# Kernel optimization log

Hardware: AMD Instinct MI355X
Metric: run time of the kernel (lower is better)

## Reference

```python
import jax, jax.numpy as jnp
import numpy as np

B, T, V, E, H, HD, L, K = 64, 512, 50000, 512, 512, 256, 2, 16
START, STOP, PAD = 13, 14, 15
NEG = -10000.0


def setup_inputs() -> dict:
    key = jax.random.key(0)
    ks = jax.random.split(key, 12)
    x = jax.random.randint(ks[0], (B, T), 0, V, dtype=jnp.int32)
    emb_table = jax.random.normal(ks[1], (V, E), jnp.float32) * 0.1
    w_ih = jax.random.normal(ks[2], (L, 2, 4 * HD, E), jnp.float32) * 0.05
    w_hh = jax.random.normal(ks[3], (L, 2, 4 * HD, HD), jnp.float32) * 0.05
    b_ih = jax.random.normal(ks[4], (L, 2, 4 * HD), jnp.float32) * 0.05
    b_hh = jax.random.normal(ks[5], (L, 2, 4 * HD), jnp.float32) * 0.05
    h0 = jax.random.normal(ks[6], (2 * L, B, HD), jnp.float32)
    c0 = jax.random.normal(ks[7], (2 * L, B, HD), jnp.float32)
    w_out = jax.random.normal(ks[8], (K, H), jnp.float32) * 0.05
    b_out = jax.random.normal(ks[9], (K,), jnp.float32) * 0.05
    t = jax.random.normal(ks[10], (K, K), jnp.float32)
    # replicate the in-place edits (order matters: pad overrides stop/start crossings)
    t = t.at[START, :].set(NEG)
    t = t.at[:, STOP].set(NEG)
    t = t.at[PAD, :].set(0.0)
    t = t.at[:, PAD].set(0.0)
    return {"x": x, "seq_len": T, "emb_table": emb_table, "w_ih": w_ih,
            "w_hh": w_hh, "b_ih": b_ih, "b_hh": b_hh, "h0": h0, "c0": c0,
            "w_out": w_out, "b_out": b_out, "transition": t}


def _lstm_dir(xs, h0, c0, Wih, Whh, b):
    # xs: [B, T, in]; single-direction LSTM, torch gate order (i, f, g, o)
    def step(carry, x_t):
        h, c = carry
        gates = x_t @ Wih.T + h @ Whh.T + b  # [B, 4*HD]
        i, f, g, o = jnp.split(gates, 4, axis=-1)
        c = jax.nn.sigmoid(f) * c + jax.nn.sigmoid(i) * jnp.tanh(g)
        h = jax.nn.sigmoid(o) * jnp.tanh(c)
        return (h, c), h
    _, hs = jax.lax.scan(step, (h0, c0), jnp.swapaxes(xs, 0, 1))  # [T, B, HD]
    return jnp.swapaxes(hs, 0, 1)


def _log_exp_sum(vec):
    # faithful to the original: per-row max over last dim, but sum of exp over ALL elements
    m = jnp.max(vec, axis=-1)
    return m + jnp.log(jnp.sum(jnp.exp(vec - m[..., None])))


def reference(x, seq_len, emb_table, w_ih, w_hh, b_ih, b_hh, h0, c0, w_out, b_out, transition):
    out = emb_table[x]  # [B, T, E]
    for l in range(L):
        fwd = _lstm_dir(out, h0[2 * l], c0[2 * l], w_ih[l, 0], w_hh[l, 0], b_ih[l, 0] + b_hh[l, 0])
        bwd = _lstm_dir(out[:, ::-1], h0[2 * l + 1], c0[2 * l + 1], w_ih[l, 1], w_hh[l, 1], b_ih[l, 1] + b_hh[l, 1])[:, ::-1]
        out = jnp.concatenate([fwd, bwd], axis=-1)  # [B, T, H]
    tag_scores = out @ w_out.T + b_out  # [B, T, K]

    # CRF forward algorithm (vectorized form of the nested time/tag loops)
    alpha0 = jnp.full((B, K), NEG, dtype=tag_scores.dtype).at[:, START].set(0.0)

    def crf_step(alpha, feat_t):  # feat_t: [B, K]
        vec = alpha[:, None, :] + feat_t[:, :, None] + transition[None, :, :]  # [B, Knext, Kprev]
        m = jnp.max(vec, axis=-1)  # [B, Knext]
        # original log_exp_sum sums exp over the whole [B, Kprev] slice per next_tag
        s = jnp.sum(jnp.exp(vec - m[..., None]), axis=(0, 2))  # [Knext]
        return m + jnp.log(s)[None, :], None

    alpha, _ = jax.lax.scan(crf_step, alpha0, jnp.swapaxes(tag_scores, 0, 1))
    terminal = alpha + transition[STOP][None, :]
    forward_score = _log_exp_sum(terminal)  # [B]
    return tag_scores, forward_score
```

## Files before the change

kernel.cpp:

```cpp
#include <hip/hip_runtime.h>

#define B_ 64
#define T_ 512
#define E_ 512
#define HD_ 256
#define H_ 512
#define K_ 16
#define NEG_ (-10000.0f)
#define START_ 13
#define STOP_ 14

typedef unsigned int u32;
using half8  = __attribute__((ext_vector_type(8))) _Float16;
using f32x4  = __attribute__((ext_vector_type(4))) float;
using half2v = __attribute__((ext_vector_type(2))) _Float16;

__device__ __forceinline__ int dot4i8(u32 a, u32 b, int c) {
#if __has_builtin(__builtin_amdgcn_sdot4)
    return __builtin_amdgcn_sdot4((int)a, (int)b, c, false);
#else
    int r = c;
#pragma unroll
    for (int i = 0; i < 4; ++i) {
        int xa = ((int)a << (24 - 8 * i)) >> 24;
        int xb = ((int)b << (24 - 8 * i)) >> 24;
        r += xa * xb;
    }
    return r;
#endif
}
__device__ __forceinline__ int dotq(uint4 w, uint4 h, int a) {
    a = dot4i8(w.x, h.x, a); a = dot4i8(w.y, h.y, a);
    a = dot4i8(w.z, h.z, a); a = dot4i8(w.w, h.w, a);
    return a;
}
__device__ __forceinline__ float sigm(float x) { return 1.f / (1.f + __expf(-x)); }
__device__ __forceinline__ float tanh_f(float x) {
    float a = fabsf(x);
    float e = __expf(-2.f * a);
    float t = (1.f - e) / (1.f + e);
    return x < 0.f ? -t : t;
}

__global__ void cvt_f16_k(const float* __restrict__ src, _Float16* __restrict__ dst, int n4) {
    int i = blockIdx.x * blockDim.x + threadIdx.x;
    if (i < n4) {
        float4 v = ((const float4*)src)[i];
        half2v a; a.x = (_Float16)v.x; a.y = (_Float16)v.y;
        half2v b; b.x = (_Float16)v.z; b.y = (_Float16)v.w;
        ((u32*)dst)[2 * i]     = __builtin_bit_cast(u32, a);
        ((u32*)dst)[2 * i + 1] = __builtin_bit_cast(u32, b);
    }
}
__global__ void bias_sum_k(const float* __restrict__ bih, const float* __restrict__ bhh,
                           float* __restrict__ bs) {
    int i = blockIdx.x * blockDim.x + threadIdx.x;
    if (i < 4096) bs[i] = bih[i] + bhh[i];
}

__global__ void quant_whh_k(const float* __restrict__ whh,
                            u32* __restrict__ wq,
                            float* __restrict__ dqw) {
    const int row = blockIdx.x, lane = threadIdx.x;
    const float4 v = ((const float4*)(whh + (size_t)row * 256))[lane];
    float m = fmaxf(fmaxf(fabsf(v.x), fabsf(v.y)), fmaxf(fabsf(v.z), fabsf(v.w)));
#pragma unroll
    for (int off = 32; off >= 1; off >>= 1) m = fmaxf(m, __shfl_xor(m, off, 64));
    m = fmaxf(m, 1e-8f);
    const float s = 127.f / m;
    int b0 = ((int)rintf(v.x * s)) & 255;
    int b1 = ((int)rintf(v.y * s)) & 255;
    int b2 = ((int)rintf(v.z * s)) & 255;
    int b3 = ((int)rintf(v.w * s)) & 255;
    wq[(size_t)row * 64 + lane] = (u32)(b0 | (b1 << 8) | (b2 << 16) | (b3 << 24));
    if (lane == 0) dqw[row] = m / (127.f * 127.f);
}

__global__ void embed_k(const int* __restrict__ x, const float* __restrict__ emb,
                        _Float16* __restrict__ xe) {
    int m = blockIdx.x;
    int row = x[m];
    int c = threadIdx.x * 4;
    float4 v = *(const float4*)(emb + (size_t)row * E_ + c);
    half2v p0; p0.x = (_Float16)v.x; p0.y = (_Float16)v.y;
    half2v p1; p1.x = (_Float16)v.z; p1.y = (_Float16)v.w;
    u32* dst = (u32*)(xe + (size_t)m * E_) + threadIdx.x * 2;
    dst[0] = __builtin_bit_cast(u32, p0);
    dst[1] = __builtin_bit_cast(u32, p1);
}

__global__ __launch_bounds__(256) void gemm_bt(const _Float16* __restrict__ A,
                                               const _Float16* __restrict__ Bw,
                                               const float* __restrict__ bsum,
                                               _Float16* __restrict__ C,
                                               int M, int N, int Kd) {
    __shared__ __align__(16) _Float16 As[128 * 64];
    __shared__ __align__(16) _Float16 Bs[128 * 64];
    const int nTn = N >> 7;
    const int tm = blockIdx.x / nTn, tn = blockIdx.x % nTn;
    const int tid = threadIdx.x;
    const int lane = tid & 63, wave = tid >> 6;
    const int wr = wave >> 1, wc = wave & 1;
    f32x4 acc[4][4];
#pragma unroll
    for (int i = 0; i < 4; ++i)
#pragma unroll
        for (int j = 0; j < 4; ++j) acc[i][j] = f32x4{0.f, 0.f, 0.f, 0.f};
    const int lr = lane & 15, lk = (lane >> 4) * 8;

    for (int k0 = 0; k0 < Kd; k0 += 64) {
#pragma unroll
        for (int r = 0; r < 4; ++r) {
            int c = r * 256 + tid;
            const _Float16* srcA = A + (size_t)(tm * 128 + (c >> 3)) * Kd + k0 + (c & 7) * 8;
            const _Float16* srcB = Bw + (size_t)(tn * 128 + (c >> 3)) * Kd + k0 + (c & 7) * 8;
            _Float16* dA = &As[(size_t)(r * 256 + wave * 64) * 8];
            _Float16* dB = &Bs[(size_t)(r * 256 + wave * 64) * 8];
            __builtin_amdgcn_global_load_lds((const __attribute__((address_space(1))) void*)srcA,
                                             (__attribute__((address_space(3))) void*)dA, 16, 0, 0);
            __builtin_amdgcn_global_load_lds((const __attribute__((address_space(1))) void*)srcB,
                                             (__attribute__((address_space(3))) void*)dB, 16, 0, 0);
        }
        __syncthreads();
#pragma unroll
        for (int kk = 0; kk < 2; ++kk) {
            half8 av[4], bv[4];
#pragma unroll
            for (int i = 0; i < 4; ++i)
                av[i] = *(const half8*)&As[(wr * 64 + i * 16 + lr) * 64 + kk * 32 + lk];
#pragma unroll
            for (int j = 0; j < 4; ++j)
                bv[j] = *(const half8*)&Bs[(wc * 64 + j * 16 + lr) * 64 + kk * 32 + lk];
#pragma unroll
            for (int i = 0; i < 4; ++i)
#pragma unroll
                for (int j = 0; j < 4; ++j)
                    acc[i][j] = __builtin_amdgcn_mfma_f32_16x16x32_f16(av[i], bv[j], acc[i][j], 0, 0, 0);
        }
        __syncthreads();
    }
    const int mq = (lane >> 4) * 4;
#pragma unroll
    for (int i = 0; i < 4; ++i)
#pragma unroll
        for (int j = 0; j < 4; ++j) {
            int m0 = tm * 128 + wr * 64 + i * 16 + mq;
            int n0 = tn * 128 + wc * 64 + j * 16 + lr;
            float bv = bsum[n0];
#pragma unroll
            for (int q = 0; q < 4; ++q)
                C[(size_t)(m0 + q) * N + n0] = (_Float16)(acc[i][j][q] + bv);
        }
}

__global__ __attribute__((amdgpu_flat_work_group_size(512, 512), amdgpu_waves_per_eu(2, 2)))
void lstm_layer_k(
    const u32* __restrict__ wq,
    const float* __restrict__ dqw,
    const float* __restrict__ h0,
    const float* __restrict__ c0,
    const _Float16* __restrict__ Z,
    _Float16* __restrict__ Hout) {
    __shared__ __align__(16) u32 hbuf[2][64];
    __shared__ float g_sh[1024];
    __shared__ float m0sh;
    const int tid = threadIdx.x;
    const int b = blockIdx.x >> 1, dir = blockIdx.x & 1;
    const int R0 = tid, R1 = tid + 512;

    const uint4* w4 = (const uint4*)(wq + (size_t)dir * 1024 * 64);
    uint4 wa[16], wb[16];
#pragma unroll
    for (int i = 0; i < 16; ++i) wa[i] = w4[(size_t)R0 * 16 + i];
#pragma unroll
    for (int i = 0; i < 16; ++i) wb[i] = w4[(size_t)R1 * 16 + i];
    const float dq0 = dqw[dir * 1024 + R0];
    const float dq1 = dqw[dir * 1024 + R1];

    float c = 0.f;
    if (tid < 256) c = c0[(size_t)dir * B_ * HD_ + b * HD_ + tid];
    if (tid < 64) {
        float4 hv = ((const float4*)(h0 + (size_t)dir * B_ * HD_ + (size_t)b * HD_))[tid];
        float am = fmaxf(fmaxf(fabsf(hv.x), fabsf(hv.y)), fmaxf(fabsf(hv.z), fabsf(hv.w)));
#pragma unroll
        for (int off = 32; off >= 1; off >>= 1) am = fmaxf(am, __shfl_xor(am, off, 64));
        am = fmaxf(am, 1e-6f);
        float sc = 127.f / am;
        int q0 = ((int)rintf(hv.x * sc)) & 255, q1 = ((int)rintf(hv.y * sc)) & 255;
        int q2 = ((int)rintf(hv.z * sc)) & 255, q3 = ((int)rintf(hv.w * sc)) & 255;
        hbuf[0][tid] = (u32)(q0 | (q1 << 8) | (q2 << 16) | (q3 << 24));
        if (tid == 0) m0sh = am;
    }
    const _Float16* Zr = Z + (size_t)b * T_ * 2048 + dir * 1024;
    const int t0 = dir ? (T_ - 1) : 0;
    float z0 = (float)Zr[(size_t)t0 * 2048 + R0];
    float z1 = (float)Zr[(size_t)t0 * 2048 + R1];
    __syncthreads();
    const float m0v = m0sh;

    for (int s = 0; s < T_; ++s) {
        const int t = dir ? (T_ - 1 - s) : s;
        float zn0 = 0.f, zn1 = 0.f;
        if (s + 1 < T_) {
            const int tn = dir ? (t - 1) : (t + 1);
            zn0 = (float)Zr[(size_t)tn * 2048 + R0];
            zn1 = (float)Zr[(size_t)tn * 2048 + R1];
        }
        const uint4* hb = (const uint4*)&hbuf[s & 1][0];
        int a0 = 0, a1 = 0;
#pragma unroll
        for (int i = 0; i < 16; ++i) {
            uint4 hv = hb[i];
            a0 = dotq(wa[i], hv, a0);
            a1 = dotq(wb[i], hv, a1);
        }
        const float sc = (s == 0) ? m0v : 1.f;
        g_sh[R0] = (float)a0 * (dq0 * sc) + z0;
        g_sh[R1] = (float)a1 * (dq1 * sc) + z1;
        z0 = zn0; z1 = zn1;
        __syncthreads();
        if (tid < 256) {
            float gi = g_sh[tid], gf = g_sh[tid + 256];
            float gg = g_sh[tid + 512], go = g_sh[tid + 768];
            c = sigm(gf) * c + sigm(gi) * tanh_f(gg);
            float h = sigm(go) * tanh_f(c);
            Hout[(size_t)(b * T_ + t) * H_ + dir * HD_ + tid] = (_Float16)h;
            ((signed char*)&hbuf[(s + 1) & 1][0])[tid] = (signed char)(int)rintf(h * 127.f);
        }
        __syncthreads();
    }
}

__global__ __launch_bounds__(256) void tag_k(const _Float16* __restrict__ Hs,
                                             const float* __restrict__ wout,
                                             const float* __restrict__ bout,
                                             float* __restrict__ out) {
    const int tid = threadIdx.x;
    const int mi = tid >> 4, kk = tid & 15;
    const int m = blockIdx.x * 16 + mi;
    const uint4* hrow = (const uint4*)(Hs + (size_t)m * H_);
    const float4* wrow = (const float4*)(wout + (size_t)kk * H_);
    float acc = 0.f;
#pragma unroll 8
    for (int i = 0; i < 64; ++i) {
        uint4 hv = hrow[i];
        float4 w0 = wrow[2 * i], w1 = wrow[2 * i + 1];
        half2v p0 = __builtin_bit_cast(half2v, hv.x), p1 = __builtin_bit_cast(half2v, hv.y);
        half2v p2 = __builtin_bit_cast(half2v, hv.z), p3 = __builtin_bit_cast(half2v, hv.w);
        acc += (float)p0.x * w0.x + (float)p0.y * w0.y + (float)p1.x * w0.z + (float)p1.y * w0.w
             + (float)p2.x * w1.x + (float)p2.y * w1.y + (float)p3.x * w1.z + (float)p3.y * w1.w;
    }
    out[(size_t)m * K_ + kk] = acc + bout[kk];
}

__global__ __launch_bounds__(1024) void crf_k(const float* __restrict__ tag,
                                              const float* __restrict__ trans,
                                              float* __restrict__ out) {
    __shared__ float albuf[2][64][17];
    const int tid = threadIdx.x;
    const int kn = tid >> 6, b = tid & 63;
    float trow[16];
#pragma unroll
    for (int kp = 0; kp < 16; ++kp) trow[kp] = trans[kn * 16 + kp];
    albuf[0][b][kn] = (kn == START_) ? 0.f : NEG_;
    __syncthreads();
    int cur = 0;
    for (int t = 0; t < T_; ++t) {
        const float feat = tag[(size_t)(b * T_ + t) * K_ + kn];
        float v[16];
        float m = -3.4e38f;
#pragma unroll
        for (int kp = 0; kp < 16; ++kp) {
            v[kp] = albuf[cur][b][kp] + trow[kp];
            m = fmaxf(m, v[kp]);
        }
        float sm = 0.f;
#pragma unroll
        for (int kp = 0; kp < 16; ++kp) sm += __expf(v[kp] - m);
#pragma unroll
        for (int off = 32; off >= 1; off >>= 1) sm += __shfl_xor(sm, off, 64);
        albuf[cur ^ 1][b][kn] = feat + m + __logf(sm);
        __syncthreads();
        cur ^= 1;
    }
    const float term = albuf[cur][b][kn] + trans[STOP_ * 16 + kn];
    albuf[cur ^ 1][b][kn] = term;
    __syncthreads();
    if (tid < 64) {
        float mb = -3.4e38f;
#pragma unroll
        for (int k2 = 0; k2 < 16; ++k2) mb = fmaxf(mb, albuf[cur ^ 1][tid][k2]);
        float p = 0.f;
#pragma unroll
        for (int k2 = 0; k2 < 16; ++k2) p += __expf(albuf[cur ^ 1][tid][k2] - mb);
#pragma unroll
        for (int off = 32; off >= 1; off >>= 1) p += __shfl_xor(p, off, 64);
        out[(size_t)B_ * T_ * K_ + tid] = mb + __logf(p);
    }
}

extern "C" void kernel_launch(void* const* d_in, const int* in_sizes, int n_in,
                              void* d_out, int out_size, void* d_ws, size_t ws_size,
                              hipStream_t stream) {
    const int*   x     = (const int*)d_in[0];
    const float* emb   = (const float*)d_in[2];
    const float* w_ih  = (const float*)d_in[3];
    const float* w_hh  = (const float*)d_in[4];
    const float* b_ih  = (const float*)d_in[5];
    const float* b_hh  = (const float*)d_in[6];
    const float* h0    = (const float*)d_in[7];
    const float* c0    = (const float*)d_in[8];
    const float* w_out = (const float*)d_in[9];
    const float* b_out = (const float*)d_in[10];
    const float* trans = (const float*)d_in[11];
    float* out = (float*)d_out;

    char* ws = (char*)d_ws;
    u32*      wq    = (u32*)ws;
    float*    dqw   = (float*)(ws + ((size_t)1 << 20));
    _Float16* wih16 = (_Float16*)(ws + ((size_t)2 << 20));
    float*    bsum  = (float*)(ws + ((size_t)6 << 20));
    _Float16* xe    = (_Float16*)(ws + ((size_t)7 << 20));
    _Float16* Zb    = (_Float16*)(ws + ((size_t)39 << 20));
    _Float16* H0b   = (_Float16*)(ws + ((size_t)167 << 20));
    if (ws_size < ((size_t)199 << 20)) return;

    quant_whh_k<<<4096, 64, 0, stream>>>(w_hh, wq, dqw);
    cvt_f16_k<<<2048, 256, 0, stream>>>(w_ih, wih16, 2097152 / 4);
    bias_sum_k<<<16, 256, 0, stream>>>(b_ih, b_hh, bsum);
    embed_k<<<B_ * T_, 128, 0, stream>>>(x, emb, xe);

    gemm_bt<<<(32768 / 128) * (2048 / 128), 256, 0, stream>>>(xe, wih16, bsum, Zb, 32768, 2048, 512);
    lstm_layer_k<<<128, 512, 0, stream>>>(wq, dqw, h0, c0, Zb, H0b);
    gemm_bt<<<(32768 / 128) * (2048 / 128), 256, 0, stream>>>(H0b, wih16 + (size_t)2048 * 512, bsum + 2048, Zb, 32768, 2048, 512);
    lstm_layer_k<<<128, 512, 0, stream>>>(wq + (size_t)2048 * 64, dqw + 2048,
                                          h0 + 2 * B_ * HD_, c0 + 2 * B_ * HD_, Zb, xe );
    tag_k<<<32768 / 16, 256, 0, stream>>>(xe, w_out, b_out, out);
    crf_k<<<1, 1024, 0, stream>>>(out, trans, out);
}
```

Before: 1.967 ms.

## Assign all four gates of a hidden unit per lane pair, drop gate smem barrier

Restructures the recurrent LSTM step so each lane computes partial dot products for all four gates (i,f,g,o) of one hidden unit over half the hidden vector, with the lane 32 apart computing the other half. The two halves are combined with a cross-lane shuffle, so the gate values no longer go through shared memory. This removes one __syncthreads per timestep and lets every thread do the cell update instead of only half of them. The cell update is now computed redundantly by both halves, and the asm barriers pin the weights in VGPRs.

```diff
diff --git a/kernel.cpp b/kernel.cpp
--- a/kernel.cpp
+++ b/kernel.cpp
@@ -162,23 +162,35 @@
     const _Float16* __restrict__ Z,
     _Float16* __restrict__ Hout) {
     __shared__ __align__(16) u32 hbuf[2][64];
-    __shared__ float g_sh[1024];
     __shared__ float m0sh;
     const int tid = threadIdx.x;
     const int b = blockIdx.x >> 1, dir = blockIdx.x & 1;
-    const int R0 = tid, R1 = tid + 512;
-
-    const uint4* w4 = (const uint4*)(wq + (size_t)dir * 1024 * 64);
-    uint4 wa[16], wb[16];
-#pragma unroll
-    for (int i = 0; i < 16; ++i) wa[i] = w4[(size_t)R0 * 16 + i];
-#pragma unroll
-    for (int i = 0; i < 16; ++i) wb[i] = w4[(size_t)R1 * 16 + i];
-    const float dq0 = dqw[dir * 1024 + R0];
-    const float dq1 = dqw[dir * 1024 + R1];
-
-    float c = 0.f;
-    if (tid < 256) c = c0[(size_t)dir * B_ * HD_ + b * HD_ + tid];
+    const int w = tid >> 6, l = tid & 63;
+    const int half = l >> 5;
+    const int v = w * 32 + (l & 31);
+
+    const u32* wbase = wq + (size_t)dir * 1024 * 64;
+    uint4 w0[8], w1[8], w2[8], w3[8];
+#pragma unroll
+    for (int k = 0; k < 8; ++k) {
+        w0[k] = ((const uint4*)(wbase + (size_t)(0 * 256 + v) * 64 + half * 32))[k];
+        w1[k] = ((const uint4*)(wbase + (size_t)(1 * 256 + v) * 64 + half * 32))[k];
+        w2[k] = ((const uint4*)(wbase + (size_t)(2 * 256 + v) * 64 + half * 32))[k];
+        w3[k] = ((const uint4*)(wbase + (size_t)(3 * 256 + v) * 64 + half * 32))[k];
+    }
+#pragma unroll
+    for (int k = 0; k < 8; ++k) {
+        asm("" : "+v"(w0[k].x), "+v"(w0[k].y), "+v"(w0[k].z), "+v"(w0[k].w));
+        asm("" : "+v"(w1[k].x), "+v"(w1[k].y), "+v"(w1[k].z), "+v"(w1[k].w));
+        asm("" : "+v"(w2[k].x), "+v"(w2[k].y), "+v"(w2[k].z), "+v"(w2[k].w));
+        asm("" : "+v"(w3[k].x), "+v"(w3[k].y), "+v"(w3[k].z), "+v"(w3[k].w));
+    }
+    const float dq0 = dqw[dir * 1024 + 0 * 256 + v];
+    const float dq1 = dqw[dir * 1024 + 1 * 256 + v];
+    const float dq2 = dqw[dir * 1024 + 2 * 256 + v];
+    const float dq3 = dqw[dir * 1024 + 3 * 256 + v];
+
+    float c = c0[(size_t)dir * B_ * HD_ + b * HD_ + v];
     if (tid < 64) {
         float4 hv = ((const float4*)(h0 + (size_t)dir * B_ * HD_ + (size_t)b * HD_))[tid];
         float am = fmaxf(fmaxf(fabsf(hv.x), fabsf(hv.y)), fmaxf(fabsf(hv.z), fabsf(hv.w)));
@@ -193,40 +205,55 @@
     }
     const _Float16* Zr = Z + (size_t)b * T_ * 2048 + dir * 1024;
     const int t0 = dir ? (T_ - 1) : 0;
-    float z0 = (float)Zr[(size_t)t0 * 2048 + R0];
-    float z1 = (float)Zr[(size_t)t0 * 2048 + R1];
+    float z0 = 0.f, z1 = 0.f, z2 = 0.f, z3 = 0.f;
+    if (half == 0) {
+        z0 = (float)Zr[(size_t)t0 * 2048 + 0 * 256 + v];
+        z1 = (float)Zr[(size_t)t0 * 2048 + 1 * 256 + v];
+        z2 = (float)Zr[(size_t)t0 * 2048 + 2 * 256 + v];
+        z3 = (float)Zr[(size_t)t0 * 2048 + 3 * 256 + v];
+    }
     __syncthreads();
     const float m0v = m0sh;
+    float dqa = dq0 * m0v, dqb = dq1 * m0v, dqc = dq2 * m0v, dqd = dq3 * m0v;
 
     for (int s = 0; s < T_; ++s) {
         const int t = dir ? (T_ - 1 - s) : s;
-        float zn0 = 0.f, zn1 = 0.f;
-        if (s + 1 < T_) {
+        float zn0 = 0.f, zn1 = 0.f, zn2 = 0.f, zn3 = 0.f;
+        if (half == 0 && s + 1 < T_) {
             const int tn = dir ? (t - 1) : (t + 1);
-            zn0 = (float)Zr[(size_t)tn * 2048 + R0];
-            zn1 = (float)Zr[(size_t)tn * 2048 + R1];
-        }
-        const uint4* hb = (const uint4*)&hbuf[s & 1][0];
-        int a0 = 0, a1 = 0;
-#pragma unroll
-        for (int i = 0; i < 16; ++i) {
-            uint4 hv = hb[i];
-            a0 = dotq(wa[i], hv, a0);
-            a1 = dotq(wb[i], hv, a1);
-        }
-        const float sc = (s == 0) ? m0v : 1.f;
-        g_sh[R0] = (float)a0 * (dq0 * sc) + z0;
-        g_sh[R1] = (float)a1 * (dq1 * sc) + z1;
-        z0 = zn0; z1 = zn1;
-        __syncthreads();
-        if (tid < 256) {
-            float gi = g_sh[tid], gf = g_sh[tid + 256];
-            float gg = g_sh[tid + 512], go = g_sh[tid + 768];
-            c = sigm(gf) * c + sigm(gi) * tanh_f(gg);
-            float h = sigm(go) * tanh_f(c);
-            Hout[(size_t)(b * T_ + t) * H_ + dir * HD_ + tid] = (_Float16)h;
-            ((signed char*)&hbuf[(s + 1) & 1][0])[tid] = (signed char)(int)rintf(h * 127.f);
-        }
+            zn0 = (float)Zr[(size_t)tn * 2048 + 0 * 256 + v];
+            zn1 = (float)Zr[(size_t)tn * 2048 + 1 * 256 + v];
+            zn2 = (float)Zr[(size_t)tn * 2048 + 2 * 256 + v];
+            zn3 = (float)Zr[(size_t)tn * 2048 + 3 * 256 + v];
+        }
+        const uint4* hb = (const uint4*)&hbuf[s & 1][half * 32];
+        uint4 hv[8];
+#pragma unroll
+        for (int k = 0; k < 8; ++k) hv[k] = hb[k];
+        int p0 = 0, p1 = 0, p2 = 0, p3 = 0;
+#pragma unroll
+        for (int k = 0; k < 8; ++k) {
+            p0 = dotq(w0[k], hv[k], p0);
+            p1 = dotq(w1[k], hv[k], p1);
+            p2 = dotq(w2[k], hv[k], p2);
+            p3 = dotq(w3[k], hv[k], p3);
+        }
+        float f0 = (float)p0 * dqa + z0;
+        float f1 = (float)p1 * dqb + z1;
+        float f2 = (float)p2 * dqc + z2;
+        float f3 = (float)p3 * dqd + z3;
+        f0 += __shfl_xor(f0, 32, 64);
+        f1 += __shfl_xor(f1, 32, 64);
+        f2 += __shfl_xor(f2, 32, 64);
+        f3 += __shfl_xor(f3, 32, 64);
+        c = sigm(f1) * c + sigm(f0) * tanh_f(f2);
+        const float h = sigm(f3) * tanh_f(c);
+        if (half == 0) {
+            Hout[(size_t)(b * T_ + t) * H_ + dir * HD_ + v] = (_Float16)h;
+            ((signed char*)&hbuf[(s + 1) & 1][0])[v] = (signed char)(int)rintf(h * 127.f);
+        }
+        if (s == 0) { dqa = dq0; dqb = dq1; dqc = dq2; dqd = dq3; }
+        z0 = zn0; z1 = zn1; z2 = zn2; z3 = zn3;
         __syncthreads();
     }
 }
```

New measurement: 2.266 ms. 1.15x slower.
